# Kernel optimization log

Hardware: AMD Instinct MI355X
Metric: run time of the kernel (lower is better)

Reference implementation:

```python
import jax, jax.numpy as jnp
import numpy as np

C, DEPTH, HEADS, WS = 180, 6, 6, 16
CR, SQ, OVR, MLP_RATIO = 3, 30, 0.5, 2.0
CC = C // CR                      # 60 compressed channels
CSE = CC // (SQ // CR)            # 6 SE squeeze channels
HID = int(C * MLP_RATIO)          # 360 mlp hidden
OWS = int(WS * (1 + OVR))         # 24 overlapping window
HD = C // HEADS                   # 30 head dim


def _rel_index(ws):
    coords = np.stack(np.meshgrid(np.arange(ws), np.arange(ws), indexing='ij')).reshape(2, -1)
    rel = (coords[:, :, None] - coords[:, None, :]).transpose(1, 2, 0)
    rel[..., 0] += ws - 1; rel[..., 1] += ws - 1; rel[..., 0] *= 2 * ws - 1
    return jnp.asarray(rel.sum(-1))

REL_IDX = _rel_index(WS)  # (WS^2, WS^2) int


def _shift_mask(H, W, ws, ss):
    m = np.zeros((H, W), np.float32); cnt = 0
    sl = (slice(0, -ws), slice(-ws, -ss), slice(-ss, None))
    for h in sl:
        for w in sl:
            m[h, w] = cnt; cnt += 1
    mw = m.reshape(H // ws, ws, W // ws, ws).transpose(0, 2, 1, 3).reshape(-1, ws * ws)
    am = mw[:, None, :] - mw[:, :, None]
    return jnp.asarray(np.where(am != 0, -100.0, 0.0).astype(np.float32))  # (nW, N, N)


def _ln(x, w, b):
    mu = x.mean(-1, keepdims=True)
    var = ((x - mu) ** 2).mean(-1, keepdims=True)
    return (x - mu) * jax.lax.rsqrt(var + 1e-5) * w + b


def _wpart(x, ws):
    B, H, W, c = x.shape
    return x.reshape(B, H // ws, ws, W // ws, ws, c).transpose(0, 1, 3, 2, 4, 5).reshape(-1, ws, ws, c)


def _wrev(w, ws, H, W):
    B = w.shape[0] // ((H // ws) * (W // ws))
    return w.reshape(B, H // ws, W // ws, ws, ws, -1).transpose(0, 1, 3, 2, 4, 5).reshape(B, H, W, -1)


def _conv(x, w, b, pad):
    y = jax.lax.conv_general_dilated(x, w, (1, 1), [(pad, pad), (pad, pad)], dimension_numbers=('NCHW', 'OIHW', 'NCHW'))
    return y + b[None, :, None, None]


def _window_msa(xw, qkv_w, qkv_b, relb, pw, pb, mask):
    Bw, N, c = xw.shape
    qkv = (xw @ qkv_w + qkv_b).reshape(Bw, N, 3, HEADS, HD).transpose(2, 0, 3, 1, 4)
    q, k, v = qkv[0], qkv[1], qkv[2]
    attn = jnp.einsum('bhqd,bhkd->bhqk', q, k) * (HD ** -0.5)
    attn = attn + relb[REL_IDX].transpose(2, 0, 1)[None]  # relative position bias (h,N,N)
    if mask is not None:
        nW = mask.shape[0]
        attn = (attn.reshape(Bw // nW, nW, HEADS, N, N) + mask[None, :, None]).reshape(Bw, HEADS, N, N)
    attn = jax.nn.softmax(attn, axis=-1)
    out = jnp.einsum('bhqk,bhkd->bhqd', attn, v).transpose(0, 2, 1, 3).reshape(Bw, N, c)
    return out @ pw + pb


def _hab(x, H, W, shift, n1w, n1b, qkvw, qkvb, relb, pw, pb, ccw, ccb, ca1w, ca1b, ca2w, ca2b, cew, ceb, n2w, n2b, m1w, m1b, m2w, m2b):
    B, N, c = x.shape
    xn = _ln(x, n1w, n1b).reshape(B, H, W, c)
    if shift > 0:
        xn = jnp.roll(xn, (-shift, -shift), (1, 2))
    mask = _shift_mask(H, W, WS, shift) if shift > 0 else None
    wins = _wpart(xn, WS).reshape(-1, WS * WS, c)
    a = _window_msa(wins, qkvw, qkvb, relb, pw, pb, mask).reshape(-1, WS, WS, c)
    xa = _wrev(a, WS, H, W)
    if shift > 0:
        xa = jnp.roll(xa, (shift, shift), (1, 2))
    x = x + xa.reshape(B, N, c)
    feat = x.transpose(0, 2, 1).reshape(B, c, H, W)
    comp = _conv(feat, ccw, ccb, 1)       # (B,CC,H,W)
    s = comp.mean((2, 3))                 # SE squeeze (B,CC)
    g = jax.nn.sigmoid(jax.nn.relu(s @ ca1w + ca1b) @ ca2w + ca2b)
    ca = _conv(comp * g[:, :, None, None], cew, ceb, 1)
    x = x + ca.reshape(B, c, N).transpose(0, 2, 1)
    h = _ln(x, n2w, n2b)
    return x + jax.nn.gelu(h @ m1w + m1b, approximate=False) @ m2w + m2b


def _ocab(x, H, W, nw, nb, qw, qb, kvw, kvb, pw, pb):
    B, N, c = x.shape
    xn = _ln(x, nw, nb)
    feat = xn.transpose(0, 2, 1).reshape(B, c, H, W)
    q = _wpart(feat.transpose(0, 2, 3, 1), WS).reshape(-1, WS * WS, c) @ qw + qb
    pad = (OWS - WS) // 2
    fp = jnp.pad(feat, ((0, 0), (0, 0), (pad, pad), (pad, pad)))
    nWh, nWw = H // WS, W // WS
    ih = (np.arange(nWh) * WS)[:, None] + np.arange(OWS)[None, :]
    iw = (np.arange(nWw) * WS)[:, None] + np.arange(OWS)[None, :]
    patches = fp[:, :, ih[:, None, :, None], iw[None, :, None, :]]   # (B,c,nWh,nWw,OWS,OWS) = unfold
    kvf = patches.transpose(0, 2, 3, 4, 5, 1).reshape(B * nWh * nWw, OWS * OWS, c)
    k, v = jnp.split(kvf @ kvw + kvb, 2, axis=-1)
    Bn = kvf.shape[0]
    qh = q.reshape(Bn, WS * WS, HEADS, HD).transpose(0, 2, 1, 3)
    kh = k.reshape(Bn, OWS * OWS, HEADS, HD).transpose(0, 2, 1, 3)
    vh = v.reshape(Bn, OWS * OWS, HEADS, HD).transpose(0, 2, 1, 3)
    attn = jax.nn.softmax(jnp.einsum('bhqd,bhkd->bhqk', qh, kh) * (HD ** -0.5), axis=-1)
    out = jnp.einsum('bhqk,bhkd->bhqd', attn, vh).transpose(0, 2, 1, 3).reshape(Bn, WS * WS, c)
    out = _wrev((out @ pw + pb).reshape(-1, WS, WS, c), WS, H, W)
    return x + out.reshape(B, N, c)


def setup_inputs() -> dict:
    ks = iter(jax.random.split(jax.random.key(0), 40))
    def nrm(shape):
        return jax.random.normal(next(ks), shape, jnp.float32) * 0.02
    D = DEPTH
    return dict(
        x=jax.random.normal(next(ks), (1, 192 * 192, C), jnp.float32),
        hab_n1_w=jnp.ones((D, C)), hab_n1_b=jnp.zeros((D, C)),
        hab_qkv_w=nrm((D, C, 3 * C)), hab_qkv_b=jnp.zeros((D, 3 * C)),
        hab_relb=nrm((D, (2 * WS - 1) ** 2, HEADS)),
        hab_proj_w=nrm((D, C, C)), hab_proj_b=jnp.zeros((D, C)),
        hab_cc_w=nrm((D, CC, C, 3, 3)), hab_cc_b=jnp.zeros((D, CC)),
        hab_ca1_w=nrm((D, CC, CSE)), hab_ca1_b=jnp.zeros((D, CSE)),
        hab_ca2_w=nrm((D, CSE, CC)), hab_ca2_b=jnp.zeros((D, CC)),
        hab_ce_w=nrm((D, C, CC, 3, 3)), hab_ce_b=jnp.zeros((D, C)),
        hab_n2_w=jnp.ones((D, C)), hab_n2_b=jnp.zeros((D, C)),
        hab_m1_w=nrm((D, C, HID)), hab_m1_b=jnp.zeros((D, HID)),
        hab_m2_w=nrm((D, HID, C)), hab_m2_b=jnp.zeros((D, C)),
        ocab_n_w=jnp.ones((C,)), ocab_n_b=jnp.zeros((C,)),
        ocab_q_w=nrm((C, C)), ocab_q_b=jnp.zeros((C,)),
        ocab_kv_w=nrm((C, 2 * C)), ocab_kv_b=jnp.zeros((2 * C,)),
        ocab_p_w=nrm((C, C)), ocab_p_b=jnp.zeros((C,)),
        conv_w=nrm((C, C, 3, 3)), conv_b=jnp.zeros((C,)),
        H=192, W=192,
    )


def reference(x, hab_n1_w, hab_n1_b, hab_qkv_w, hab_qkv_b, hab_relb, hab_proj_w, hab_proj_b, hab_cc_w, hab_cc_b, hab_ca1_w, hab_ca1_b, hab_ca2_w, hab_ca2_b, hab_ce_w, hab_ce_b, hab_n2_w, hab_n2_b, hab_m1_w, hab_m1_b, hab_m2_w, hab_m2_b, ocab_n_w, ocab_n_b, ocab_q_w, ocab_q_b, ocab_kv_w, ocab_kv_b, ocab_p_w, ocab_p_b, conv_w, conv_b, H, W):
    B, N, c = x.shape
    shortcut = x
    for i in range(DEPTH):
        shift = 0 if i % 2 == 0 else WS // 2
        x = _hab(x, H, W, shift, hab_n1_w[i], hab_n1_b[i], hab_qkv_w[i], hab_qkv_b[i], hab_relb[i], hab_proj_w[i], hab_proj_b[i], hab_cc_w[i], hab_cc_b[i], hab_ca1_w[i], hab_ca1_b[i], hab_ca2_w[i], hab_ca2_b[i], hab_ce_w[i], hab_ce_b[i], hab_n2_w[i], hab_n2_b[i], hab_m1_w[i], hab_m1_b[i], hab_m2_w[i], hab_m2_b[i])
    x = _ocab(x, H, W, ocab_n_w, ocab_n_b, ocab_q_w, ocab_q_b, ocab_kv_w, ocab_kv_b, ocab_p_w, ocab_p_b)
    feat = _conv(x.transpose(0, 2, 1).reshape(B, c, H, W), conv_w, conv_b, 1)
    return shortcut + feat.reshape(B, c, N).transpose(0, 2, 1)
```

## Files before the change

kernel.cpp:

```cpp
#include <hip/hip_runtime.h>
#include <math.h>


#define DEV __device__ __forceinline__

constexpr int HH   = 192;
constexpr int WW   = 192;
constexpr int NT   = HH * WW;
constexpr int C    = 180;
constexpr int HEADS= 6;
constexpr int HD   = 30;
constexpr int WS   = 16;
constexpr int NWW  = WW / WS;
constexpr int NWIN = 144;
constexpr int NTW  = 256;
constexpr int OWS  = 24;
constexpr int NKV  = OWS*OWS;
constexpr int CCH  = 60;
constexpr int CSE  = 6;
constexpr int HID  = 360;
constexpr int DEPTH= 6;

typedef _Float16 h8   __attribute__((ext_vector_type(8)));
typedef _Float16 h4   __attribute__((ext_vector_type(4)));
typedef float    f32x4 __attribute__((ext_vector_type(4)));

constexpr int PKG = 2048;
constexpr int PKC = 18432;

constexpr int QKV_PL = 9*6*PKG;
constexpr int PROJ_PL= 3*6*PKG;
constexpr int M1_PL  = 6*6*PKG;
constexpr int M2_PL  = 3*12*PKG;
constexpr int OQ_PL  = 3*6*PKG;
constexpr int OKV_PL = 6*6*PKG;
constexpr int OP_PL  = 3*6*PKG;
constexpr int CC_PL  = 1*6*PKC;
constexpr int CE_PL  = 3*2*PKC;
constexpr int FIN_PL = 3*6*PKC;

constexpr size_t PO_QKV = 0;
constexpr size_t PO_PROJ= PO_QKV + 6ull*QKV_PL;
constexpr size_t PO_M1  = PO_PROJ+ 6ull*PROJ_PL;
constexpr size_t PO_M2  = PO_M1  + 6ull*M1_PL;
constexpr size_t PO_OQ  = PO_M2  + 6ull*M2_PL;
constexpr size_t PO_OKV = PO_OQ  + OQ_PL;
constexpr size_t PO_OP  = PO_OKV + OKV_PL;
constexpr size_t PO_CC  = PO_OP  + OP_PL;
constexpr size_t PO_CE  = PO_CC  + 6ull*CC_PL;
constexpr size_t PO_FIN = PO_CE  + 6ull*CE_PL;
constexpr size_t PK_HALFS = PO_FIN + FIN_PL;

constexpr size_t OFF_X    = 0;
constexpr size_t OFF_A    = OFF_X    + (size_t)NT*C;
constexpr size_t OFF_B    = OFF_A    + (size_t)NT*C;
constexpr size_t OFF_COMP = OFF_B    + (size_t)NT*C;
constexpr size_t OFF_S    = OFF_COMP + (size_t)NT*CCH;
constexpr size_t OFF_G    = OFF_S    + 64;
constexpr size_t OFF_QKV  = OFF_G    + 64;
constexpr size_t OFF_PK   = OFF_QKV  + 16000000;
constexpr size_t OFF_PB   = OFF_PK   + PK_HALFS/2 + 8;

DEV int win_to_nat(int r, int shift) {
  int w   = r >> 8;
  int pos = r & 255;
  int wh = w / NWW, ww = w - wh*NWW;
  int rh = wh*WS + (pos >> 4);
  int rw = ww*WS + (pos & 15);
  int sh = rh + shift; if (sh >= HH) sh -= HH;
  int sw = rw + shift; if (sw >= WW) sw -= WW;
  return sh*WW + sw;
}

DEV int ocab_src_row(int gr) {
  int w = gr / NKV;
  int t = gr - w*NKV;
  int wh = w / NWW, ww = w - wh*NWW;
  int i = t / OWS, j = t - i*OWS;
  int gh = wh*WS - 4 + i;
  int gw = ww*WS - 4 + j;
  if ((unsigned)gh >= (unsigned)HH || (unsigned)gw >= (unsigned)WW) return -1;
  return (((gh >> 4)*NWW + (gw >> 4)) << 8) + ((gh & 15) << 4) + (gw & 15);
}

DEV float gelu_exact(float v) {
  return 0.5f * v * (1.0f + erff(v * 0.70710678118654752f));
}

DEV int col_remap(int np, int mode) {
  if (mode == 0) return np;
  int d = np & 31, hh = (np >> 5) % 6;
  if (d >= 30) return -1;
  if (mode == 1) { int third = np / 192; return third*180 + hh*30 + d; }
  if (mode == 2) { int half  = np / 192; return half *180 + hh*30 + d; }
  return hh*30 + d;
}

__global__ __launch_bounds__(256) void pack_gemmw(
    const float* __restrict__ W, _Float16* __restrict__ Wp,
    int K, int N, int nch, int mode, float scale,
    int perLayer, int nlayers, int sstride)
{
  int idx = blockIdx.x * 256 + threadIdx.x;
  if (idx >= perLayer * nlayers) return;
  int layer = idx / perLayer;
  int rem = idx - layer*perLayer;
  int unit = rem >> 11;
  int r2 = rem & 2047;
  int nb = r2 >> 9;
  int lane = (r2 >> 3) & 63;
  int j = r2 & 7;
  int cb = unit / nch, ch = unit - cb*nch;
  int quad = lane >> 4, l16 = lane & 15;
  int np = cb*64 + nb*16 + l16;
  int gk = ch*32 + quad*8 + j;
  float v = 0.f;
  if (gk < K) {
    int sc = col_remap(np, mode);
    if (sc >= 0 && sc < N)
      v = W[(size_t)layer*sstride + (size_t)gk*N + sc] * scale;
  }
  Wp[idx] = (_Float16)v;
}

__global__ __launch_bounds__(256) void pack_bias(
    const float* __restrict__ b, float* __restrict__ bp,
    int N, int Np, int mode, float scale, int nlayers)
{
  int idx = blockIdx.x * 256 + threadIdx.x;
  if (idx >= Np * nlayers) return;
  int layer = idx / Np, np = idx - layer*Np;
  int sc = col_remap(np, mode);
  bp[idx] = (sc >= 0 && sc < N) ? b[layer*N + sc] * scale : 0.f;
}

__global__ __launch_bounds__(256) void pack_convw(
    const float* __restrict__ Wc, _Float16* __restrict__ Wp,
    int IC, int OC, int nch, int perLayer, int nlayers, int sstride)
{
  int idx = blockIdx.x * 256 + threadIdx.x;
  if (idx >= perLayer * nlayers) return;
  int layer = idx / perLayer;
  int rem = idx - layer*perLayer;
  int unit = rem / PKC;
  int w2 = rem - unit*PKC;
  int tap = w2 >> 11;
  int r2 = w2 & 2047;
  int nb = r2 >> 9;
  int lane = (r2 >> 3) & 63;
  int j = r2 & 7;
  int cb = unit / nch, ch = unit - cb*nch;
  int quad = lane >> 4, l16 = lane & 15;
  int oc = cb*64 + nb*16 + l16;
  int gk = ch*32 + quad*8 + j;
  float v = 0.f;
  if (oc < OC && gk < IC)
    v = Wc[(size_t)layer*sstride + ((size_t)oc * IC + gk) * 9 + tap];
  Wp[idx] = (_Float16)v;
}

__global__ __launch_bounds__(256) void ln2_kernel(
    const float* __restrict__ X, const float* __restrict__ gw,
    const float* __restrict__ gb, _Float16* __restrict__ OUT,
    int mode, int shift)
{
  int wave = threadIdx.x >> 6, lane = threadIdx.x & 63;
  int r = blockIdx.x * 4 + wave;
  int s = (mode == 1) ? win_to_nat(r, shift) : r;
  const float* xr = X + (size_t)s * C;
  float v0 = xr[lane];
  float v1 = xr[lane + 64];
  float v2 = (lane < C - 128) ? xr[lane + 128] : 0.f;
  float sum = v0 + v1 + v2;
  float sq  = v0*v0 + v1*v1 + v2*v2;
  #pragma unroll
  for (int off = 32; off > 0; off >>= 1) {
    sum += __shfl_down(sum, off);
    sq  += __shfl_down(sq,  off);
  }
  sum = __shfl(sum, 0);
  sq  = __shfl(sq,  0);
  float mu  = sum * (1.f / C);
  float var = sq * (1.f / C) - mu * mu;
  float inv = rsqrtf(var + 1e-5f);
  _Float16* orow = OUT + (size_t)r * 192;
  orow[lane]      = (_Float16)((v0 - mu) * inv * gw[lane]      + gb[lane]);
  orow[lane + 64] = (_Float16)((v1 - mu) * inv * gw[lane + 64] + gb[lane + 64]);
  if (lane < C - 128)
    orow[lane + 128] = (_Float16)((v2 - mu) * inv * gw[lane + 128] + gb[lane + 128]);
  if (lane < 12) orow[180 + lane] = (_Float16)0.f;
}

__global__ __launch_bounds__(256) void gemm2(
    const _Float16* __restrict__ A, int lda,
    const _Float16* __restrict__ Wp, const float* __restrict__ bias,
    _Float16* __restrict__ O16, int ldo, int nstore,
    float* __restrict__ O32, const float* __restrict__ RES,
    int K, int nch, int amap, int emap, int epi, int shift)
{
  __shared__ _Float16 As[128][40];
  int tid  = threadIdx.x;
  int lane = tid & 63, wave = tid >> 6;
  int quad = lane >> 4, ln16 = lane & 15;
  int row0 = blockIdx.y * 128;
  int col0 = blockIdx.x * 64;

  f32x4 acc[2][4];
  #pragma unroll
  for (int mt = 0; mt < 2; ++mt)
    #pragma unroll
    for (int nb = 0; nb < 4; ++nb)
      #pragma unroll
      for (int r = 0; r < 4; ++r) acc[mt][nb][r] = 0.f;

  const _Float16* wlane = Wp + (size_t)lane*8;

  for (int c = 0; c < nch; ++c) {
    int k0 = c * 32;
    if (c) __syncthreads();
    #pragma unroll
    for (int i = 0; i < 2; ++i) {
      int task = i*256 + tid;
      int ar = task >> 2, ak = (task & 3) * 8;
      int gr = row0 + ar;
      int sr = amap ? ocab_src_row(gr) : gr;
      h8 av;
      #pragma unroll
      for (int j = 0; j < 8; ++j) av[j] = (_Float16)0.f;
      if (sr >= 0) {
        const _Float16* ap = A + (size_t)sr*lda + k0 + ak;
        if (k0 + ak + 8 <= K) av = *(const h8*)ap;
        else {
          #pragma unroll
          for (int j = 0; j < 8; ++j)
            if (k0 + ak + j < K) av[j] = ap[j];
        }
      }
      *(h8*)&As[ar][ak] = av;
    }
    h8 bf[4];
    #pragma unroll
    for (int nb = 0; nb < 4; ++nb)
      bf[nb] = *(const h8*)(wlane + (size_t)(blockIdx.x*nch + c)*PKG + (size_t)nb*512);
    __syncthreads();
    h8 af0 = *(const h8*)&As[wave*32 + ln16][quad*8];
    h8 af1 = *(const h8*)&As[wave*32 + 16 + ln16][quad*8];
    #pragma unroll
    for (int nb = 0; nb < 4; ++nb) {
      acc[0][nb] = __builtin_amdgcn_mfma_f32_16x16x32_f16(af0, bf[nb], acc[0][nb], 0, 0, 0);
      acc[1][nb] = __builtin_amdgcn_mfma_f32_16x16x32_f16(af1, bf[nb], acc[1][nb], 0, 0, 0);
    }
  }

  #pragma unroll
  for (int mt = 0; mt < 2; ++mt)
    #pragma unroll
    for (int r = 0; r < 4; ++r) {
      int m = row0 + wave*32 + mt*16 + quad*4 + r;
      int dst = emap ? win_to_nat(m, shift) : m;
      #pragma unroll
      for (int nb = 0; nb < 4; ++nb) {
        int n = col0 + nb*16 + ln16;
        if (n < nstore) {
          float v = acc[mt][nb][r] + bias[n];
          if (epi == 2) {
            v += RES[(size_t)dst*180 + n];
            O32[(size_t)dst*180 + n] = v;
          } else {
            if (epi == 1) v = gelu_exact(v);
            O16[(size_t)dst*ldo + n] = (_Float16)v;
          }
        }
      }
    }
}

__global__ __launch_bounds__(256) void conv9_mfma(
    const float* __restrict__ Xf, const _Float16* __restrict__ Xh, int ldah,
    const _Float16* __restrict__ Wp, const float* __restrict__ bias,
    const float* __restrict__ scale, const float* __restrict__ RES,
    float* __restrict__ O32, _Float16* __restrict__ O16,
    int IC, int OC, int nch)
{
  __shared__ _Float16 hs[3][66][40];
  int tid  = threadIdx.x;
  int lane = tid & 63, wave = tid >> 6;
  int quad = lane >> 4, ln16 = lane & 15;
  int p0 = blockIdx.y * 64;
  int h  = p0 / WW;
  int w0 = p0 - h * WW;
  int col0 = blockIdx.x * 64;

  f32x4 acc[4];
  #pragma unroll
  for (int nb = 0; nb < 4; ++nb)
    #pragma unroll
    for (int r = 0; r < 4; ++r) acc[nb][r] = 0.f;

  for (int c = 0; c < nch; ++c) {
    int k0 = c * 32;
    if (c) __syncthreads();
    for (int idx = tid; idx < 3*66*4; idx += 256) {
      int r    = idx / (66*4);
      int rem  = idx - r*(66*4);
      int px   = rem >> 2;
      int ks   = (rem & 3) * 8;
      int gh = h - 1 + r, gw = w0 - 1 + px;
      h8 hv;
      #pragma unroll
      for (int j = 0; j < 8; ++j) hv[j] = (_Float16)0.f;
      if ((unsigned)gh < (unsigned)HH && (unsigned)gw < (unsigned)WW) {
        if (Xh) {
          const _Float16* sp = Xh + (size_t)(gh*WW + gw) * ldah + k0 + ks;
          h8 t = *(const h8*)sp;
          if (scale) {
            #pragma unroll
            for (int j = 0; j < 8; ++j)
              hv[j] = (_Float16)((float)t[j] * scale[k0 + ks + j]);
          } else hv = t;
        } else {
          const float* sp = Xf + (size_t)(gh*WW + gw) * IC + k0 + ks;
          if (k0 + ks + 8 <= IC) {
            float4 q0 = *(const float4*)sp;
            float4 q1 = *(const float4*)(sp + 4);
            hv[0]=(_Float16)q0.x; hv[1]=(_Float16)q0.y; hv[2]=(_Float16)q0.z; hv[3]=(_Float16)q0.w;
            hv[4]=(_Float16)q1.x; hv[5]=(_Float16)q1.y; hv[6]=(_Float16)q1.z; hv[7]=(_Float16)q1.w;
          } else {
            #pragma unroll
            for (int j = 0; j < 8; ++j)
              if (k0 + ks + j < IC) hv[j] = (_Float16)sp[j];
          }
        }
      }
      *(h8*)&hs[r][px][ks] = hv;
    }
    __syncthreads();

    const _Float16* wpc = Wp + (size_t)(blockIdx.x*nch + c) * PKC + (size_t)lane*8;
    h8 bf[4];
    #pragma unroll
    for (int nb = 0; nb < 4; ++nb)
      bf[nb] = *(const h8*)(wpc + (size_t)nb*512);
    #pragma unroll
    for (int tap = 0; tap < 9; ++tap) {
      h8 bfn[4];
      if (tap < 8) {
        #pragma unroll
        for (int nb = 0; nb < 4; ++nb)
          bfn[nb] = *(const h8*)(wpc + (size_t)(tap+1)*2048 + (size_t)nb*512);
      }
      int dyy = tap / 3, dxt = tap - dyy*3;
      h8 af = *(const h8*)&hs[dyy][wave*16 + ln16 + dxt][quad*8];
      #pragma unroll
      for (int nb = 0; nb < 4; ++nb)
        acc[nb] = __builtin_amdgcn_mfma_f32_16x16x32_f16(af, bf[nb], acc[nb], 0, 0, 0);
      if (tap < 8) {
        #pragma unroll
        for (int nb = 0; nb < 4; ++nb) bf[nb] = bfn[nb];
      }
    }
  }

  #pragma unroll
  for (int r = 0; r < 4; ++r) {
    int p = p0 + wave*16 + quad*4 + r;
    #pragma unroll
    for (int nb = 0; nb < 4; ++nb) {
      int oc = col0 + nb*16 + ln16;
      if (O16) {
        float v = (oc < OC) ? acc[nb][r] + bias[oc] : 0.f;
        O16[(size_t)p*64 + oc] = (_Float16)v;
      } else if (oc < OC) {
        float v = acc[nb][r] + bias[oc] + RES[(size_t)p * OC + oc];
        O32[(size_t)p * OC + oc] = v;
      }
    }
  }
}

__global__ __launch_bounds__(256) void win_attn_mfma(
    const _Float16* __restrict__ QKV, const float* __restrict__ relb,
    _Float16* __restrict__ OUT, int shift)
{
  __shared__ _Float16 Kf[256][40];
  __shared__ _Float16 Vt[32][264];
  __shared__ _Float16 rbs[962];
  __shared__ unsigned char rg[256];
  int b = blockIdx.x;
  int w = b / HEADS, hd = b - (b / HEADS)*HEADS;
  int tid = threadIdx.x, lane = tid & 63, wave = tid >> 6;
  int quad = lane >> 4, ln16 = lane & 15;
  const _Float16* base = QKV + (size_t)(w*NTW)*576;

  #pragma unroll
  for (int i = 0; i < 4; ++i) {
    int task = i*256 + tid;
    int row = task >> 2, seg = (task & 3) * 8;
    *(h8*)&Kf[row][seg] = *(const h8*)(base + (size_t)row*576 + 192 + hd*32 + seg);
    h8 hv = *(const h8*)(base + (size_t)row*576 + 384 + hd*32 + seg);
    #pragma unroll
    for (int j = 0; j < 8; ++j) Vt[seg + j][row] = hv[j];
  }
  for (int i = tid; i < 961; i += 256) rbs[i] = (_Float16)relb[i*HEADS + hd];
  if (shift > 0) {
    int wh = w / NWW, ww = w - wh*NWW;
    int rh = wh*WS + (tid >> 4), rw = ww*WS + (tid & 15);
    int regh = (rh < HH - WS) ? 0 : (rh < HH - 8 ? 1 : 2);
    int regw = (rw < WW - WS) ? 0 : (rw < WW - 8 ? 1 : 2);
    rg[tid] = (unsigned char)(regh*3 + regw);
  }

  h8 bq[4];
  #pragma unroll
  for (int qi = 0; qi < 4; ++qi) {
    int q = wave*64 + qi*16 + ln16;
    bq[qi] = *(const h8*)(base + (size_t)q*576 + hd*32 + quad*8);
  }
  __syncthreads();

  float mrun[4], lrun[4];
  f32x4 accO[4][2];
  #pragma unroll
  for (int qi = 0; qi < 4; ++qi) {
    mrun[qi] = -1e30f; lrun[qi] = 0.f;
    #pragma unroll
    for (int r = 0; r < 4; ++r) { accO[qi][0][r] = 0.f; accO[qi][1][r] = 0.f; }
  }
  int rgq[4] = {0,0,0,0};
  if (shift > 0) {
    #pragma unroll
    for (int qi = 0; qi < 4; ++qi) rgq[qi] = rg[wave*64 + qi*16 + ln16];
  }
  const f32x4 zero4 = {0.f,0.f,0.f,0.f};

  for (int kb = 0; kb < 4; ++kb) {
    f32x4 st[4][4];
    #pragma unroll
    for (int kt = 0; kt < 4; ++kt) {
      h8 ak = *(const h8*)&Kf[kb*64 + kt*16 + ln16][quad*8];
      #pragma unroll
      for (int qi = 0; qi < 4; ++qi)
        st[kt][qi] = __builtin_amdgcn_mfma_f32_16x16x32_f16(ak, bq[qi], zero4, 0, 0, 0);
    }
    #pragma unroll
    for (int qi = 0; qi < 4; ++qi) {
      int q = wave*64 + qi*16 + ln16;
      int qrr = q >> 4, qcc = q & 15;
      float bmax = -1e30f;
      #pragma unroll
      for (int kt = 0; kt < 4; ++kt) {
        int bidx0 = (qrr - (kb*4 + kt) + 15)*31 + qcc + 15 - quad*4;
        #pragma unroll
        for (int r = 0; r < 4; ++r) {
          float s = st[kt][qi][r] + (float)rbs[bidx0 - r];
          if (shift > 0) {
            int key = kb*64 + kt*16 + quad*4 + r;
            if (rg[key] != rgq[qi]) s -= 100.f;
          }
          st[kt][qi][r] = s;
          bmax = fmaxf(bmax, s);
        }
      }
      bmax = fmaxf(bmax, __shfl_xor(bmax, 16));
      bmax = fmaxf(bmax, __shfl_xor(bmax, 32));
      float mnew  = fmaxf(mrun[qi], bmax);
      float alpha = __expf(mrun[qi] - mnew);
      mrun[qi] = mnew;
      float ps = 0.f;
      #pragma unroll
      for (int kt = 0; kt < 4; ++kt)
        #pragma unroll
        for (int r = 0; r < 4; ++r) {
          float p = __expf(st[kt][qi][r] - mnew);
          st[kt][qi][r] = p; ps += p;
        }
      ps += __shfl_xor(ps, 16);
      ps += __shfl_xor(ps, 32);
      lrun[qi] = lrun[qi]*alpha + ps;
      #pragma unroll
      for (int r = 0; r < 4; ++r) {
        float fr = __shfl(alpha, quad*4 + r);
        accO[qi][0][r] *= fr;
        accO[qi][1][r] *= fr;
      }
    }
    #pragma unroll
    for (int kt = 0; kt < 4; ++kt) {
      int kbase = kb*64 + kt*16 + quad*4;
      h4 bv0 = *(const h4*)&Vt[ln16][kbase];
      h4 bv1 = *(const h4*)&Vt[16 + ln16][kbase];
      #pragma unroll
      for (int qi = 0; qi < 4; ++qi) {
        h4 ap;
        #pragma unroll
        for (int j = 0; j < 4; ++j) ap[j] = (_Float16)st[kt][qi][j];
        accO[qi][0] = __builtin_amdgcn_mfma_f32_16x16x16f16(ap, bv0, accO[qi][0], 0, 0, 0);
        accO[qi][1] = __builtin_amdgcn_mfma_f32_16x16x16f16(ap, bv1, accO[qi][1], 0, 0, 0);
      }
    }
  }

  #pragma unroll
  for (int qi = 0; qi < 4; ++qi) {
    float linv = 1.f / lrun[qi];
    #pragma unroll
    for (int r = 0; r < 4; ++r) {
      float fr = __shfl(linv, quad*4 + r);
      int q = wave*64 + qi*16 + quad*4 + r;
      _Float16* o = OUT + (size_t)(w*NTW + q)*192 + hd*HD;
      o[ln16] = (_Float16)(accO[qi][0][r] * fr);
      if (ln16 < HD - 16) o[16 + ln16] = (_Float16)(accO[qi][1][r] * fr);
    }
  }
}

__global__ __launch_bounds__(256) void ocab_attn_mfma(
    const _Float16* __restrict__ Q, const _Float16* __restrict__ KV,
    _Float16* __restrict__ OUT)
{
  constexpr int CH = 192;
  __shared__ _Float16 Kf[CH][40];
  __shared__ _Float16 Vt[32][200];
  int b = blockIdx.x;
  int w = b / HEADS, hd = b - (b / HEADS)*HEADS;
  int tid = threadIdx.x, lane = tid & 63, wave = tid >> 6;
  int quad = lane >> 4, ln16 = lane & 15;

  h8 bq[4];
  #pragma unroll
  for (int qi = 0; qi < 4; ++qi) {
    int q = wave*64 + qi*16 + ln16;
    bq[qi] = *(const h8*)(Q + (size_t)(w*NTW + q)*192 + hd*32 + quad*8);
  }

  float mrun[4], lrun[4];
  f32x4 accO[4][2];
  #pragma unroll
  for (int qi = 0; qi < 4; ++qi) {
    mrun[qi] = -1e30f; lrun[qi] = 0.f;
    #pragma unroll
    for (int r = 0; r < 4; ++r) { accO[qi][0][r] = 0.f; accO[qi][1][r] = 0.f; }
  }
  const f32x4 zero4 = {0.f,0.f,0.f,0.f};

  for (int ch = 0; ch < 3; ++ch) {
    __syncthreads();
    #pragma unroll
    for (int i = 0; i < 3; ++i) {
      int task = i*256 + tid;
      int row = task >> 2, seg = (task & 3) * 8;
      const _Float16* kvr = KV + (size_t)(w*NKV + ch*CH + row)*384;
      *(h8*)&Kf[row][seg] = *(const h8*)(kvr + hd*32 + seg);
      h8 hv = *(const h8*)(kvr + 192 + hd*32 + seg);
      #pragma unroll
      for (int j = 0; j < 8; ++j) Vt[seg + j][row] = hv[j];
    }
    __syncthreads();

    for (int kb = 0; kb < 3; ++kb) {
      f32x4 st[4][4];
      #pragma unroll
      for (int kt = 0; kt < 4; ++kt) {
        h8 ak = *(const h8*)&Kf[kb*64 + kt*16 + ln16][quad*8];
        #pragma unroll
        for (int qi = 0; qi < 4; ++qi)
          st[kt][qi] = __builtin_amdgcn_mfma_f32_16x16x32_f16(ak, bq[qi], zero4, 0, 0, 0);
      }
      #pragma unroll
      for (int qi = 0; qi < 4; ++qi) {
        float bmax = -1e30f;
        #pragma unroll
        for (int kt = 0; kt < 4; ++kt)
          #pragma unroll
          for (int r = 0; r < 4; ++r) bmax = fmaxf(bmax, st[kt][qi][r]);
        bmax = fmaxf(bmax, __shfl_xor(bmax, 16));
        bmax = fmaxf(bmax, __shfl_xor(bmax, 32));
        float mnew  = fmaxf(mrun[qi], bmax);
        float alpha = __expf(mrun[qi] - mnew);
        mrun[qi] = mnew;
        float ps = 0.f;
        #pragma unroll
        for (int kt = 0; kt < 4; ++kt)
          #pragma unroll
          for (int r = 0; r < 4; ++r) {
            float p = __expf(st[kt][qi][r] - mnew);
            st[kt][qi][r] = p; ps += p;
          }
        ps += __shfl_xor(ps, 16);
        ps += __shfl_xor(ps, 32);
        lrun[qi] = lrun[qi]*alpha + ps;
        #pragma unroll
        for (int r = 0; r < 4; ++r) {
          float fr = __shfl(alpha, quad*4 + r);
          accO[qi][0][r] *= fr;
          accO[qi][1][r] *= fr;
        }
      }
      #pragma unroll
      for (int kt = 0; kt < 4; ++kt) {
        int kbase = kb*64 + kt*16 + quad*4;
        h4 bv0 = *(const h4*)&Vt[ln16][kbase];
        h4 bv1 = *(const h4*)&Vt[16 + ln16][kbase];
        #pragma unroll
        for (int qi = 0; qi < 4; ++qi) {
          h4 ap;
          #pragma unroll
          for (int j = 0; j < 4; ++j) ap[j] = (_Float16)st[kt][qi][j];
          accO[qi][0] = __builtin_amdgcn_mfma_f32_16x16x16f16(ap, bv0, accO[qi][0], 0, 0, 0);
          accO[qi][1] = __builtin_amdgcn_mfma_f32_16x16x16f16(ap, bv1, accO[qi][1], 0, 0, 0);
        }
      }
    }
  }

  #pragma unroll
  for (int qi = 0; qi < 4; ++qi) {
    float linv = 1.f / lrun[qi];
    #pragma unroll
    for (int r = 0; r < 4; ++r) {
      float fr = __shfl(linv, quad*4 + r);
      int q = wave*64 + qi*16 + quad*4 + r;
      _Float16* o = OUT + (size_t)(w*NTW + q)*192 + hd*HD;
      o[ln16] = (_Float16)(accO[qi][0][r] * fr);
      if (ln16 < HD - 16) o[16 + ln16] = (_Float16)(accO[qi][1][r] * fr);
    }
  }
}

__global__ __launch_bounds__(256) void colsum_kernel(
    const _Float16* __restrict__ COMP, float* __restrict__ S)
{
  int tid = threadIdx.x;
  int seg = tid & 7, rb = tid >> 3;
  int row0 = blockIdx.x * 128;
  float a[8] = {};
  #pragma unroll
  for (int i = 0; i < 4; ++i) {
    int row = row0 + i*32 + rb;
    h8 v = *(const h8*)(COMP + (size_t)row*64 + seg*8);
    #pragma unroll
    for (int j = 0; j < 8; ++j) a[j] += (float)v[j];
  }
  __shared__ float sA[64];
  if (tid < 64) sA[tid] = 0.f;
  __syncthreads();
  #pragma unroll
  for (int j = 0; j < 8; ++j) atomicAdd(&sA[seg*8 + j], a[j]);
  __syncthreads();
  if (tid < 60) atomicAdd(&S[tid], sA[tid]);
}

__global__ __launch_bounds__(64) void se_kernel(
    const float* __restrict__ S, const float* __restrict__ w1,
    const float* __restrict__ b1, const float* __restrict__ w2,
    const float* __restrict__ b2, float* __restrict__ G)
{
  __shared__ float hid[CSE];
  int t = threadIdx.x;
  if (t < CSE) {
    float a = b1[t];
    for (int c = 0; c < CCH; ++c) a += (S[c] * (1.f/NT)) * w1[c * CSE + t];
    hid[t] = fmaxf(a, 0.f);
  }
  __syncthreads();
  if (t < CCH) {
    float a = b2[t];
    #pragma unroll
    for (int j = 0; j < CSE; ++j) a += hid[j] * w2[j * CCH + t];
    G[t] = 1.f / (1.f + __expf(-a));
  }
}


extern "C" void kernel_launch(void* const* d_in, const int* in_sizes, int n_in,
                              void* d_out, int out_size, void* d_ws, size_t ws_size,
                              hipStream_t stream) {
  const float* x_in   = (const float*)d_in[0];
  const float* n1w    = (const float*)d_in[1];
  const float* n1b    = (const float*)d_in[2];
  const float* qkvw   = (const float*)d_in[3];
  const float* qkvb   = (const float*)d_in[4];
  const float* relb   = (const float*)d_in[5];
  const float* projw  = (const float*)d_in[6];
  const float* projb  = (const float*)d_in[7];
  const float* ccw    = (const float*)d_in[8];
  const float* ccb    = (const float*)d_in[9];
  const float* ca1w   = (const float*)d_in[10];
  const float* ca1b   = (const float*)d_in[11];
  const float* ca2w   = (const float*)d_in[12];
  const float* ca2b   = (const float*)d_in[13];
  const float* cew    = (const float*)d_in[14];
  const float* ceb    = (const float*)d_in[15];
  const float* n2w    = (const float*)d_in[16];
  const float* n2b    = (const float*)d_in[17];
  const float* m1w    = (const float*)d_in[18];
  const float* m1b    = (const float*)d_in[19];
  const float* m2w    = (const float*)d_in[20];
  const float* m2b    = (const float*)d_in[21];
  const float* onw    = (const float*)d_in[22];
  const float* onb    = (const float*)d_in[23];
  const float* oqw    = (const float*)d_in[24];
  const float* oqb    = (const float*)d_in[25];
  const float* okvw   = (const float*)d_in[26];
  const float* okvb   = (const float*)d_in[27];
  const float* opw    = (const float*)d_in[28];
  const float* opb    = (const float*)d_in[29];
  const float* convw  = (const float*)d_in[30];
  const float* convb  = (const float*)d_in[31];

  float* ws   = (float*)d_ws;
  float*     X    = ws + OFF_X;
  _Float16*  A    = (_Float16*)(ws + OFF_A);
  _Float16*  Bq   = (_Float16*)(ws + OFF_B);
  _Float16*  COMP = (_Float16*)(ws + OFF_COMP);
  float*     S    = ws + OFF_S;
  float*     G    = ws + OFF_G;
  _Float16*  QKV  = (_Float16*)(ws + OFF_QKV);
  _Float16*  PK   = (_Float16*)(ws + OFF_PK);
  float*     PB   = ws + OFF_PB;

  float* qkvB = PB;
  float* oqB  = PB + 6*576;
  float* okvB = oqB + 192;

  const float scl = 0.18257418583505536f;

  (void)hipMemcpyAsync(X, x_in, (size_t)NT * C * sizeof(float),
                       hipMemcpyDeviceToDevice, stream);

  #define GRID(n) dim3(((n)+255)/256)
  pack_gemmw<<<GRID(6*QKV_PL), 256, 0, stream>>>(qkvw, PK+PO_QKV, 180, 540, 6, 1, 1.f, QKV_PL, 6, 180*540);
  pack_gemmw<<<GRID(6*PROJ_PL),256, 0, stream>>>(projw, PK+PO_PROJ,180, 180, 6, 0, 1.f, PROJ_PL,6, 180*180);
  pack_gemmw<<<GRID(6*M1_PL), 256, 0, stream>>>(m1w,  PK+PO_M1,  180, 360, 6, 0, 1.f, M1_PL,  6, 180*360);
  pack_gemmw<<<GRID(6*M2_PL), 256, 0, stream>>>(m2w,  PK+PO_M2,  360, 180,12, 0, 1.f, M2_PL,  6, 360*180);
  pack_gemmw<<<GRID(OQ_PL),   256, 0, stream>>>(oqw,  PK+PO_OQ,  180, 180, 6, 3, scl, OQ_PL,  1, 0);
  pack_gemmw<<<GRID(OKV_PL),  256, 0, stream>>>(okvw, PK+PO_OKV, 180, 360, 6, 2, 1.f, OKV_PL, 1, 0);
  pack_gemmw<<<GRID(OP_PL),   256, 0, stream>>>(opw,  PK+PO_OP,  180, 180, 6, 0, 1.f, OP_PL,  1, 0);
  pack_convw<<<GRID(6*CC_PL), 256, 0, stream>>>(ccw,  PK+PO_CC,  180,  60, 6, CC_PL, 6, 60*180*9);
  pack_convw<<<GRID(6*CE_PL), 256, 0, stream>>>(cew,  PK+PO_CE,   60, 180, 2, CE_PL, 6, 180*60*9);
  pack_convw<<<GRID(FIN_PL),  256, 0, stream>>>(convw,PK+PO_FIN, 180, 180, 6, FIN_PL,1, 0);
  pack_bias<<<GRID(6*576), 256, 0, stream>>>(qkvb, qkvB, 540, 576, 1, 1.f, 6);
  pack_bias<<<GRID(192),   256, 0, stream>>>(oqb,  oqB,  180, 192, 3, scl, 1);
  pack_bias<<<GRID(384),   256, 0, stream>>>(okvb, okvB, 360, 384, 2, 1.f, 1);

  const int MB128 = NT / 128;
  const int MB64  = NT / 64;

  for (int i = 0; i < DEPTH; ++i) {
    int shift = (i % 2 == 0) ? 0 : WS / 2;
    ln2_kernel<<<NT/4, 256, 0, stream>>>(X, n1w + i*C, n1b + i*C, A, 1, shift);
    gemm2<<<dim3(9, MB128), 256, 0, stream>>>(
        A, 192, PK+PO_QKV + (size_t)i*QKV_PL, qkvB + i*576,
        QKV, 576, 576, nullptr, nullptr, 180, 6, 0, 0, 0, 0);
    win_attn_mfma<<<NWIN*HEADS, 256, 0, stream>>>(
        QKV, relb + (size_t)i*961*HEADS, A, shift);
    gemm2<<<dim3(3, MB128), 256, 0, stream>>>(
        A, 192, PK+PO_PROJ + (size_t)i*PROJ_PL, projb + i*C,
        nullptr, 0, 180, X, X, 180, 6, 0, 1, 2, shift);
    conv9_mfma<<<dim3(1, MB64), 256, 0, stream>>>(
        X, nullptr, 0, PK+PO_CC + (size_t)i*CC_PL, ccb + i*CCH,
        nullptr, nullptr, nullptr, COMP, 180, 60, 6);
    (void)hipMemsetAsync(S, 0, 64*sizeof(float), stream);
    colsum_kernel<<<288, 256, 0, stream>>>(COMP, S);
    se_kernel<<<1, 64, 0, stream>>>(
        S, ca1w + (size_t)i*CCH*CSE, ca1b + (size_t)i*CSE,
        ca2w + (size_t)i*CSE*CCH, ca2b + (size_t)i*CCH, G);
    conv9_mfma<<<dim3(3, MB64), 256, 0, stream>>>(
        nullptr, COMP, 64, PK+PO_CE + (size_t)i*CE_PL, ceb + i*C,
        G, X, X, nullptr, 60, 180, 2);
    ln2_kernel<<<NT/4, 256, 0, stream>>>(X, n2w + i*C, n2b + i*C, A, 0, 0);
    gemm2<<<dim3(6, MB128), 256, 0, stream>>>(
        A, 192, PK+PO_M1 + (size_t)i*M1_PL, m1b + i*HID,
        QKV, 384, 360, nullptr, nullptr, 180, 6, 0, 0, 1, 0);
    gemm2<<<dim3(3, MB128), 256, 0, stream>>>(
        QKV, 384, PK+PO_M2 + (size_t)i*M2_PL, m2b + i*C,
        nullptr, 0, 180, X, X, 360, 12, 0, 0, 2, 0);
  }

  ln2_kernel<<<NT/4, 256, 0, stream>>>(X, onw, onb, A, 1, 0);
  gemm2<<<dim3(3, MB128), 256, 0, stream>>>(
      A, 192, PK+PO_OQ, oqB, Bq, 192, 192, nullptr, nullptr, 180, 6, 0, 0, 0, 0);
  gemm2<<<dim3(6, NWIN*NKV/128), 256, 0, stream>>>(
      A, 192, PK+PO_OKV, okvB, QKV, 384, 384, nullptr, nullptr, 180, 6, 1, 0, 0, 0);
  ocab_attn_mfma<<<NWIN*HEADS, 256, 0, stream>>>(Bq, QKV, A);
  gemm2<<<dim3(3, MB128), 256, 0, stream>>>(
      A, 192, PK+PO_OP, opb, nullptr, 0, 180, X, X, 180, 6, 0, 1, 2, 0);

  conv9_mfma<<<dim3(3, MB64), 256, 0, stream>>>(
      X, nullptr, 0, PK+PO_FIN, convb, nullptr, x_in,
      (float*)d_out, nullptr, 180, 180, 6);
}
```

Measured before the change: 2.483 ms.

## Keep fp16 mirror of residual stream, stage full K in gemm, 2-row conv tiles

New measurement: 3.253 ms. 1.31x slower.

```diff
diff --git a/kernel.cpp b/kernel.cpp
--- a/kernel.cpp
+++ b/kernel.cpp
@@ -60,6 +60,7 @@
 constexpr size_t OFF_QKV  = OFF_G    + 64;
 constexpr size_t OFF_PK   = OFF_QKV  + 16000000;
 constexpr size_t OFF_PB   = OFF_PK   + PK_HALFS/2 + 8;
+constexpr size_t OFF_X16  = OFF_PB   + 4096;
 
 DEV int win_to_nat(int r, int shift) {
   int w   = r >> 8;
@@ -159,18 +160,37 @@
   Wp[idx] = (_Float16)v;
 }
 
+__global__ __launch_bounds__(256) void initx_kernel(
+    const float* __restrict__ x_in, float* __restrict__ X,
+    _Float16* __restrict__ X16)
+{
+  int wave = threadIdx.x >> 6, lane = threadIdx.x & 63;
+  int r = blockIdx.x * 4 + wave;
+  const float* xr = x_in + (size_t)r * C;
+  float v0 = xr[lane];
+  float v1 = xr[lane + 64];
+  float v2 = (lane < 52) ? xr[lane + 128] : 0.f;
+  float* xo = X + (size_t)r * C;
+  xo[lane] = v0; xo[lane + 64] = v1;
+  if (lane < 52) xo[lane + 128] = v2;
+  _Float16* m = X16 + (size_t)r * 192;
+  m[lane] = (_Float16)v0; m[lane + 64] = (_Float16)v1;
+  if (lane < 52) m[lane + 128] = (_Float16)v2;
+  if (lane < 12) m[180 + lane] = (_Float16)0.f;
+}
+
 __global__ __launch_bounds__(256) void ln2_kernel(
-    const float* __restrict__ X, const float* __restrict__ gw,
+    const _Float16* __restrict__ Xh, const float* __restrict__ gw,
     const float* __restrict__ gb, _Float16* __restrict__ OUT,
     int mode, int shift)
 {
   int wave = threadIdx.x >> 6, lane = threadIdx.x & 63;
   int r = blockIdx.x * 4 + wave;
   int s = (mode == 1) ? win_to_nat(r, shift) : r;
-  const float* xr = X + (size_t)s * C;
-  float v0 = xr[lane];
-  float v1 = xr[lane + 64];
-  float v2 = (lane < C - 128) ? xr[lane + 128] : 0.f;
+  const _Float16* xr = Xh + (size_t)s * 192;
+  float v0 = (float)xr[lane];
+  float v1 = (float)xr[lane + 64];
+  float v2 = (lane < 52) ? (float)xr[lane + 128] : 0.f;
   float sum = v0 + v1 + v2;
   float sq  = v0*v0 + v1*v1 + v2*v2;
   #pragma unroll
@@ -186,7 +206,7 @@
   _Float16* orow = OUT + (size_t)r * 192;
   orow[lane]      = (_Float16)((v0 - mu) * inv * gw[lane]      + gb[lane]);
   orow[lane + 64] = (_Float16)((v1 - mu) * inv * gw[lane + 64] + gb[lane + 64]);
-  if (lane < C - 128)
+  if (lane < 52)
     orow[lane + 128] = (_Float16)((v2 - mu) * inv * gw[lane + 128] + gb[lane + 128]);
   if (lane < 12) orow[180 + lane] = (_Float16)0.f;
 }
@@ -196,9 +216,10 @@
     const _Float16* __restrict__ Wp, const float* __restrict__ bias,
     _Float16* __restrict__ O16, int ldo, int nstore,
     float* __restrict__ O32, const float* __restrict__ RES,
+    _Float16* __restrict__ XM,
     int K, int nch, int amap, int emap, int epi, int shift)
 {
-  __shared__ _Float16 As[128][40];
+  __shared__ _Float16 As[128][200];
   int tid  = threadIdx.x;
   int lane = tid & 63, wave = tid >> 6;
   int quad = lane >> 4, ln16 = lane & 15;
@@ -214,41 +235,47 @@
       for (int r = 0; r < 4; ++r) acc[mt][nb][r] = 0.f;
 
   const _Float16* wlane = Wp + (size_t)lane*8;
-
-  for (int c = 0; c < nch; ++c) {
-    int k0 = c * 32;
-    if (c) __syncthreads();
-    #pragma unroll
-    for (int i = 0; i < 2; ++i) {
+  int nsc = (K + 191) / 192;
+
+  for (int sc = 0; sc < nsc; ++sc) {
+    int kb = sc * 192;
+    if (sc) __syncthreads();
+    #pragma unroll
+    for (int i = 0; i < 12; ++i) {
       int task = i*256 + tid;
-      int ar = task >> 2, ak = (task & 3) * 8;
+      int ar = task / 24, seg = task - ar*24;
+      int gk = kb + seg*8;
       int gr = row0 + ar;
       int sr = amap ? ocab_src_row(gr) : gr;
       h8 av;
       #pragma unroll
       for (int j = 0; j < 8; ++j) av[j] = (_Float16)0.f;
-      if (sr >= 0) {
-        const _Float16* ap = A + (size_t)sr*lda + k0 + ak;
-        if (k0 + ak + 8 <= K) av = *(const h8*)ap;
+      if (sr >= 0 && gk < K) {
+        const _Float16* ap = A + (size_t)sr*lda + gk;
+        if (gk + 8 <= K) av = *(const h8*)ap;
         else {
           #pragma unroll
           for (int j = 0; j < 8; ++j)
-            if (k0 + ak + j < K) av[j] = ap[j];
+            if (gk + j < K) av[j] = ap[j];
         }
       }
-      *(h8*)&As[ar][ak] = av;
-    }
-    h8 bf[4];
-    #pragma unroll
-    for (int nb = 0; nb < 4; ++nb)
-      bf[nb] = *(const h8*)(wlane + (size_t)(blockIdx.x*nch + c)*PKG + (size_t)nb*512);
+      *(h8*)&As[ar][seg*8] = av;
+    }
     __syncthreads();
-    h8 af0 = *(const h8*)&As[wave*32 + ln16][quad*8];
-    h8 af1 = *(const h8*)&As[wave*32 + 16 + ln16][quad*8];
-    #pragma unroll
-    for (int nb = 0; nb < 4; ++nb) {
-      acc[0][nb] = __builtin_amdgcn_mfma_f32_16x16x32_f16(af0, bf[nb], acc[0][nb], 0, 0, 0);
-      acc[1][nb] = __builtin_amdgcn_mfma_f32_16x16x32_f16(af1, bf[nb], acc[1][nb], 0, 0, 0);
+    #pragma unroll
+    for (int c = 0; c < 6; ++c) {
+      int cglob = sc*6 + c;
+      h8 bf[4];
+      #pragma unroll
+      for (int nb = 0; nb < 4; ++nb)
+        bf[nb] = *(const h8*)(wlane + (size_t)(blockIdx.x*nch + cglob)*PKG + (size_t)nb*512);
+      h8 af0 = *(const h8*)&As[wave*32 + ln16][c*32 + quad*8];
+      h8 af1 = *(const h8*)&As[wave*32 + 16 + ln16][c*32 + quad*8];
+      #pragma unroll
+      for (int nb = 0; nb < 4; ++nb) {
+        acc[0][nb] = __builtin_amdgcn_mfma_f32_16x16x32_f16(af0, bf[nb], acc[0][nb], 0, 0, 0);
+        acc[1][nb] = __builtin_amdgcn_mfma_f32_16x16x32_f16(af1, bf[nb], acc[1][nb], 0, 0, 0);
+      }
     }
   }
 
@@ -266,6 +293,7 @@
           if (epi == 2) {
             v += RES[(size_t)dst*180 + n];
             O32[(size_t)dst*180 + n] = v;
+            XM[(size_t)dst*192 + n] = (_Float16)v;
           } else {
             if (epi == 1) v = gelu_exact(v);
             O16[(size_t)dst*ldo + n] = (_Float16)v;
@@ -276,60 +304,48 @@
 }
 
 __global__ __launch_bounds__(256) void conv9_mfma(
-    const float* __restrict__ Xf, const _Float16* __restrict__ Xh, int ldah,
+    const _Float16* __restrict__ Xh, int ldah,
     const _Float16* __restrict__ Wp, const float* __restrict__ bias,
     const float* __restrict__ scale, const float* __restrict__ RES,
-    float* __restrict__ O32, _Float16* __restrict__ O16,
-    int IC, int OC, int nch)
-{
-  __shared__ _Float16 hs[3][66][40];
+    float* __restrict__ O32, _Float16* __restrict__ XM,
+    _Float16* __restrict__ O16, int OC, int nch)
+{
+  __shared__ _Float16 hs[4][66][40];
   int tid  = threadIdx.x;
   int lane = tid & 63, wave = tid >> 6;
   int quad = lane >> 4, ln16 = lane & 15;
-  int p0 = blockIdx.y * 64;
-  int h  = p0 / WW;
-  int w0 = p0 - h * WW;
+  int by = blockIdx.y;
+  int rp = by / 3, wb = by - rp*3;
+  int h0 = rp*2;
+  int w0 = wb*64;
   int col0 = blockIdx.x * 64;
 
-  f32x4 acc[4];
-  #pragma unroll
-  for (int nb = 0; nb < 4; ++nb)
-    #pragma unroll
-    for (int r = 0; r < 4; ++r) acc[nb][r] = 0.f;
+  f32x4 acc[2][4];
+  #pragma unroll
+  for (int mt = 0; mt < 2; ++mt)
+    #pragma unroll
+    for (int nb = 0; nb < 4; ++nb)
+      #pragma unroll
+      for (int r = 0; r < 4; ++r) acc[mt][nb][r] = 0.f;
 
   for (int c = 0; c < nch; ++c) {
     int k0 = c * 32;
     if (c) __syncthreads();
-    for (int idx = tid; idx < 3*66*4; idx += 256) {
-      int r    = idx / (66*4);
-      int rem  = idx - r*(66*4);
+    for (int idx = tid; idx < 4*66*4; idx += 256) {
+      int r    = idx / 264;
+      int rem  = idx - r*264;
       int px   = rem >> 2;
       int ks   = (rem & 3) * 8;
-      int gh = h - 1 + r, gw = w0 - 1 + px;
+      int gh = h0 - 1 + r, gw = w0 - 1 + px;
       h8 hv;
       #pragma unroll
       for (int j = 0; j < 8; ++j) hv[j] = (_Float16)0.f;
       if ((unsigned)gh < (unsigned)HH && (unsigned)gw < (unsigned)WW) {
-        if (Xh) {
-          const _Float16* sp = Xh + (size_t)(gh*WW + gw) * ldah + k0 + ks;
-          h8 t = *(const h8*)sp;
-          if (scale) {
-            #pragma unroll
-            for (int j = 0; j < 8; ++j)
-              hv[j] = (_Float16)((float)t[j] * scale[k0 + ks + j]);
-          } else hv = t;
-        } else {
-          const float* sp = Xf + (size_t)(gh*WW + gw) * IC + k0 + ks;
-          if (k0 + ks + 8 <= IC) {
-            float4 q0 = *(const float4*)sp;
-            float4 q1 = *(const float4*)(sp + 4);
-            hv[0]=(_Float16)q0.x; hv[1]=(_Float16)q0.y; hv[2]=(_Float16)q0.z; hv[3]=(_Float16)q0.w;
-            hv[4]=(_Float16)q1.x; hv[5]=(_Float16)q1.y; hv[6]=(_Float16)q1.z; hv[7]=(_Float16)q1.w;
-          } else {
-            #pragma unroll
-            for (int j = 0; j < 8; ++j)
-              if (k0 + ks + j < IC) hv[j] = (_Float16)sp[j];
-          }
+        hv = *(const h8*)(Xh + (size_t)(gh*WW + gw) * ldah + k0 + ks);
+        if (scale) {
+          #pragma unroll
+          for (int j = 0; j < 8; ++j)
+            hv[j] = (_Float16)((float)hv[j] * scale[k0 + ks + j]);
         }
       }
       *(h8*)&hs[r][px][ks] = hv;
@@ -350,10 +366,13 @@
           bfn[nb] = *(const h8*)(wpc + (size_t)(tap+1)*2048 + (size_t)nb*512);
       }
       int dyy = tap / 3, dxt = tap - dyy*3;
-      h8 af = *(const h8*)&hs[dyy][wave*16 + ln16 + dxt][quad*8];
-      #pragma unroll
-      for (int nb = 0; nb < 4; ++nb)
-        acc[nb] = __builtin_amdgcn_mfma_f32_16x16x32_f16(af, bf[nb], acc[nb], 0, 0, 0);
+      h8 af0 = *(const h8*)&hs[dyy][wave*16 + ln16 + dxt][quad*8];
+      h8 af1 = *(const h8*)&hs[dyy + 1][wave*16 + ln16 + dxt][quad*8];
+      #pragma unroll
+      for (int nb = 0; nb < 4; ++nb) {
+        acc[0][nb] = __builtin_amdgcn_mfma_f32_16x16x32_f16(af0, bf[nb], acc[0][nb], 0, 0, 0);
+        acc[1][nb] = __builtin_amdgcn_mfma_f32_16x16x32_f16(af1, bf[nb], acc[1][nb], 0, 0, 0);
+      }
       if (tap < 8) {
         #pragma unroll
         for (int nb = 0; nb < 4; ++nb) bf[nb] = bfn[nb];
@@ -362,20 +381,23 @@
   }
 
   #pragma unroll
-  for (int r = 0; r < 4; ++r) {
-    int p = p0 + wave*16 + quad*4 + r;
-    #pragma unroll
-    for (int nb = 0; nb < 4; ++nb) {
-      int oc = col0 + nb*16 + ln16;
-      if (O16) {
-        float v = (oc < OC) ? acc[nb][r] + bias[oc] : 0.f;
-        O16[(size_t)p*64 + oc] = (_Float16)v;
-      } else if (oc < OC) {
-        float v = acc[nb][r] + bias[oc] + RES[(size_t)p * OC + oc];
-        O32[(size_t)p * OC + oc] = v;
-      }
-    }
-  }
+  for (int mt = 0; mt < 2; ++mt)
+    #pragma unroll
+    for (int r = 0; r < 4; ++r) {
+      int p = (h0 + mt)*WW + w0 + wave*16 + quad*4 + r;
+      #pragma unroll
+      for (int nb = 0; nb < 4; ++nb) {
+        int oc = col0 + nb*16 + ln16;
+        if (O16) {
+          float v = (oc < OC) ? acc[mt][nb][r] + bias[oc] : 0.f;
+          O16[(size_t)p*64 + oc] = (_Float16)v;
+        } else if (oc < OC) {
+          float v = acc[mt][nb][r] + bias[oc] + RES[(size_t)p * OC + oc];
+          O32[(size_t)p * OC + oc] = v;
+          if (XM) XM[(size_t)p*192 + oc] = (_Float16)v;
+        }
+      }
+    }
 }
 
 __global__ __launch_bounds__(256) void win_attn_mfma(
@@ -718,6 +740,7 @@
   _Float16*  QKV  = (_Float16*)(ws + OFF_QKV);
   _Float16*  PK   = (_Float16*)(ws + OFF_PK);
   float*     PB   = ws + OFF_PB;
+  _Float16*  X16  = (_Float16*)(ws + OFF_X16);
 
   float* qkvB = PB;
   float* oqB  = PB + 6*576;
@@ -725,8 +748,7 @@
 
   const float scl = 0.18257418583505536f;
 
-  (void)hipMemcpyAsync(X, x_in, (size_t)NT * C * sizeof(float),
-                       hipMemcpyDeviceToDevice, stream);
+  initx_kernel<<<NT/4, 256, 0, stream>>>(x_in, X, X16);
 
   #define GRID(n) dim3(((n)+255)/256)
   pack_gemmw<<<GRID(6*QKV_PL), 256, 0, stream>>>(qkvw, PK+PO_QKV, 180, 540, 6, 1, 1.f, QKV_PL, 6, 180*540);
@@ -744,49 +766,49 @@
   pack_bias<<<GRID(384),   256, 0, stream>>>(okvb, okvB, 360, 384, 2, 1.f, 1);
 
   const int MB128 = NT / 128;
-  const int MB64  = NT / 64;
+  const int CB    = 288;
 
   for (int i = 0; i < DEPTH; ++i) {
     int shift = (i % 2 == 0) ? 0 : WS / 2;
-    ln2_kernel<<<NT/4, 256, 0, stream>>>(X, n1w + i*C, n1b + i*C, A, 1, shift);
+    ln2_kernel<<<NT/4, 256, 0, stream>>>(X16, n1w + i*C, n1b + i*C, A, 1, shift);
     gemm2<<<dim3(9, MB128), 256, 0, stream>>>(
         A, 192, PK+PO_QKV + (size_t)i*QKV_PL, qkvB + i*576,
-        QKV, 576, 576, nullptr, nullptr, 180, 6, 0, 0, 0, 0);
+        QKV, 576, 576, nullptr, nullptr, nullptr, 180, 6, 0, 0, 0, 0);
     win_attn_mfma<<<NWIN*HEADS, 256, 0, stream>>>(
         QKV, relb + (size_t)i*961*HEADS, A, shift);
     gemm2<<<dim3(3, MB128), 256, 0, stream>>>(
         A, 192, PK+PO_PROJ + (size_t)i*PROJ_PL, projb + i*C,
-        nullptr, 0, 180, X, X, 180, 6, 0, 1, 2, shift);
-    conv9_mfma<<<dim3(1, MB64), 256, 0, stream>>>(
-        X, nullptr, 0, PK+PO_CC + (size_t)i*CC_PL, ccb + i*CCH,
-        nullptr, nullptr, nullptr, COMP, 180, 60, 6);
+        nullptr, 0, 180, X, X, X16, 180, 6, 0, 1, 2, shift);
+    conv9_mfma<<<dim3(1, CB), 256, 0, stream>>>(
+        X16, 192, PK+PO_CC + (size_t)i*CC_PL, ccb + i*CCH,
+        nullptr, nullptr, nullptr, nullptr, COMP, 60, 6);
     (void)hipMemsetAsync(S, 0, 64*sizeof(float), stream);
     colsum_kernel<<<288, 256, 0, stream>>>(COMP, S);
     se_kernel<<<1, 64, 0, stream>>>(
         S, ca1w + (size_t)i*CCH*CSE, ca1b + (size_t)i*CSE,
         ca2w + (size_t)i*CSE*CCH, ca2b + (size_t)i*CCH, G);
-    conv9_mfma<<<dim3(3, MB64), 256, 0, stream>>>(
-        nullptr, COMP, 64, PK+PO_CE + (size_t)i*CE_PL, ceb + i*C,
-        G, X, X, nullptr, 60, 180, 2);
-    ln2_kernel<<<NT/4, 256, 0, stream>>>(X, n2w + i*C, n2b + i*C, A, 0, 0);
+    conv9_mfma<<<dim3(3, CB), 256, 0, stream>>>(
+        COMP, 64, PK+PO_CE + (size_t)i*CE_PL, ceb + i*C,
+        G, X, X, X16, nullptr, 180, 2);
+    ln2_kernel<<<NT/4, 256, 0, stream>>>(X16, n2w + i*C, n2b + i*C, A, 0, 0);
     gemm2<<<dim3(6, MB128), 256, 0, stream>>>(
         A, 192, PK+PO_M1 + (size_t)i*M1_PL, m1b + i*HID,
-        QKV, 384, 360, nullptr, nullptr, 180, 6, 0, 0, 1, 0);
+        QKV, 384, 360, nullptr, nullptr, nullptr, 180, 6, 0, 0, 1, 0);
     gemm2<<<dim3(3, MB128), 256, 0, stream>>>(
         QKV, 384, PK+PO_M2 + (size_t)i*M2_PL, m2b + i*C,
-        nullptr, 0, 180, X, X, 360, 12, 0, 0, 2, 0);
-  }
-
-  ln2_kernel<<<NT/4, 256, 0, stream>>>(X, onw, onb, A, 1, 0);
+        nullptr, 0, 180, X, X, X16, 360, 12, 0, 0, 2, 0);
+  }
+
+  ln2_kernel<<<NT/4, 256, 0, stream>>>(X16, onw, onb, A, 1, 0);
   gemm2<<<dim3(3, MB128), 256, 0, stream>>>(
-      A, 192, PK+PO_OQ, oqB, Bq, 192, 192, nullptr, nullptr, 180, 6, 0, 0, 0, 0);
+      A, 192, PK+PO_OQ, oqB, Bq, 192, 192, nullptr, nullptr, nullptr, 180, 6, 0, 0, 0, 0);
   gemm2<<<dim3(6, NWIN*NKV/128), 256, 0, stream>>>(
-      A, 192, PK+PO_OKV, okvB, QKV, 384, 384, nullptr, nullptr, 180, 6, 1, 0, 0, 0);
+      A, 192, PK+PO_OKV, okvB, QKV, 384, 384, nullptr, nullptr, nullptr, 180, 6, 1, 0, 0, 0);
   ocab_attn_mfma<<<NWIN*HEADS, 256, 0, stream>>>(Bq, QKV, A);
   gemm2<<<dim3(3, MB128), 256, 0, stream>>>(
-      A, 192, PK+PO_OP, opb, nullptr, 0, 180, X, X, 180, 6, 0, 1, 2, 0);
-
-  conv9_mfma<<<dim3(3, MB64), 256, 0, stream>>>(
-      X, nullptr, 0, PK+PO_FIN, convb, nullptr, x_in,
-      (float*)d_out, nullptr, 180, 180, 6);
-}
+      A, 192, PK+PO_OP, opb, nullptr, 0, 180, X, X, X16, 180, 6, 0, 1, 2, 0);
+
+  conv9_mfma<<<dim3(3, CB), 256, 0, stream>>>(
+      X16, 192, PK+PO_FIN, convb, nullptr, x_in,
+      (float*)d_out, nullptr, nullptr, 180, 6);
+}
```
